# Optimization experiments

Measured on AMD Instinct MI355X. Metric: run time of the kernel, lower is better.

The kernel has to match this reference:

```python
import jax, jax.numpy as jnp
import numpy as np

N_NODES = 100000
N_EDGES = 1600000
F_IN = 64
HIDDEN = 64
N_CLASSES = 2


def setup_inputs() -> dict:
    key = jax.random.key(0)
    k1, k2, k3, k4, k5, k6 = jax.random.split(key, 6)
    x = jax.random.normal(k1, (N_NODES, F_IN), dtype=jnp.float32)
    edge_index = jax.random.randint(k2, (2, N_EDGES), 0, N_NODES, dtype=jnp.int64)
    # Glorot-ish init for GCNConv linear weights, zero bias (PyG default)
    W1 = jax.random.normal(k3, (F_IN, HIDDEN), dtype=jnp.float32) * (1.0 / np.sqrt(F_IN))
    b1 = jnp.zeros((HIDDEN,), dtype=jnp.float32)
    W2 = jax.random.normal(k4, (HIDDEN, N_CLASSES), dtype=jnp.float32) * (1.0 / np.sqrt(HIDDEN))
    b2 = jnp.zeros((N_CLASSES,), dtype=jnp.float32)
    return {"x": x, "edge_index": edge_index, "W1": W1, "b1": b1, "W2": W2, "b2": b2}


def _gcn_norm(edge_index, num_nodes):
    # Add self-loops, then symmetric normalization D^-1/2 (A+I) D^-1/2
    loops = jnp.arange(num_nodes, dtype=edge_index.dtype)
    row = jnp.concatenate([edge_index[0], loops])  # [E+N] targets
    col = jnp.concatenate([edge_index[1], loops])  # [E+N] sources
    deg = jax.ops.segment_sum(jnp.ones(row.shape[0], jnp.float32), row, num_segments=num_nodes)
    dinv = jnp.where(deg > 0, jax.lax.rsqrt(deg), 0.0)
    norm = dinv[row] * dinv[col]  # [E+N]
    return row, col, norm


def _gcn_conv(x, W, b, row, col, norm, num_nodes):
    h = x @ W                                   # [N, out]
    msg = h[col] * norm[:, None]                # gather + scale, [E+N, out]
    agg = jax.ops.segment_sum(msg, row, num_segments=num_nodes)  # scatter-add
    return agg + b


def reference(x, edge_index, W1, b1, W2, b2):
    n = x.shape[0]
    row, col, norm = _gcn_norm(edge_index, n)
    h = jax.nn.relu(_gcn_conv(x, W1, b1, row, col, norm, n))
    # dropout p=0.5 is identity in eval mode
    logits = _gcn_conv(h, W2, b2, row, col, norm, n)
    return jax.nn.softmax(logits, axis=1)
```

## Files before the change

### kernel.cpp

```cpp
#include <hip/hip_runtime.h>
#include <hip/hip_fp16.h>


typedef _Float16 f16x8 __attribute__((ext_vector_type(8)));
typedef float f32x4 __attribute__((ext_vector_type(4)));
typedef float f32x2 __attribute__((ext_vector_type(2)));

#define CAPSH 12
#define CAP (1 << CAPSH)
#define NBK 784

__device__ __forceinline__ unsigned char pack_fp8(float v) {
    return (unsigned char)(__builtin_amdgcn_cvt_pk_fp8_f32(v, 0.f, 0, false) & 0xFF);
}

__device__ __forceinline__ void unpack8_fp8(uint2 w, float* f) {
    f32x2 a = __builtin_amdgcn_cvt_pk_f32_fp8(w.x, false);
    f32x2 b = __builtin_amdgcn_cvt_pk_f32_fp8(w.x, true);
    f32x2 c = __builtin_amdgcn_cvt_pk_f32_fp8(w.y, false);
    f32x2 d = __builtin_amdgcn_cvt_pk_f32_fp8(w.y, true);
    f[0] = a.x; f[1] = a.y; f[2] = b.x; f[3] = b.y;
    f[4] = c.x; f[5] = c.y; f[6] = d.x; f[7] = d.y;
}

__global__ __launch_bounds__(256, 4) void k_binfused(const int* __restrict__ row,
                                                     const int* __restrict__ col,
                                                     int* __restrict__ relcur,
                                                     unsigned* __restrict__ pairbuf,
                                                     unsigned char* __restrict__ hp8,
                                                     const float* __restrict__ x,
                                                     const float* __restrict__ W1,
                                                     int E, int nb, int N, int nTileB) {
    __shared__ unsigned items[4096];
    __shared__ unsigned short bktid[4096];
    __shared__ int cnt[NBK];
    __shared__ int start0[NBK];
    __shared__ int cursor[NBK];
    __shared__ int gbase[NBK];

    int tid = threadIdx.x;

    if (blockIdx.x < nTileB) {
        int base = blockIdx.x * 4096;
        int m = E - base; if (m > 4096) m = 4096;

        for (int t = tid; t < nb; t += 256) cnt[t] = 0;
        __syncthreads();
        for (int i = tid; i < m; i += 256) atomicAdd(&cnt[row[base + i] >> 7], 1);
        __syncthreads();
        if (tid < 64) {
            int lane = tid, running = 0;
            for (int ch = 0; ch < 13; ++ch) {
                int idx = ch * 64 + lane;
                int v = (idx < nb) ? cnt[idx] : 0;
                int s = v;
#pragma unroll
                for (int off = 1; off < 64; off <<= 1) {
                    int t = __shfl_up(s, off, 64);
                    if (lane >= off) s += t;
                }
                if (idx < nb) { start0[idx] = running + s - v; cursor[idx] = running + s - v; }
                running += __shfl(s, 63, 64);
            }
        }
        __syncthreads();
        for (int i = tid; i < m; i += 256) {
            int r = row[base + i];
            int c = col[base + i];
            int b = r >> 7;
            int pos = atomicAdd(&cursor[b], 1);
            items[pos] = ((unsigned)(r & 127) << 24) | (unsigned)c;
            bktid[pos] = (unsigned short)b;
        }
        __syncthreads();
        for (int t = tid; t < nb; t += 256) {
            int cv = cnt[t];
            if (cv > 0) gbase[t] = (t << CAPSH) + atomicAdd(&relcur[t], cv);
        }
        __syncthreads();
        for (int i = tid; i < m; i += 256) {
            int b = bktid[i];
            pairbuf[gbase[b] + (i - start0[b])] = items[i];
        }
        if (blockIdx.x == 0 && tid < 16) ((int*)(hp8 + (size_t)N * 64))[tid] = 0;
    } else {
        int g = blockIdx.x - nTileB;
        int n0 = g << 8;
        int lane = tid & 63, q = lane >> 4, mm = lane & 15;
        f16x8 bf[4][2];
#pragma unroll
        for (int nt = 0; nt < 4; ++nt)
#pragma unroll
            for (int kk = 0; kk < 2; ++kk)
#pragma unroll
                for (int j = 0; j < 8; ++j)
                    bf[nt][kk][j] = (_Float16)W1[(kk * 32 + q * 8 + j) * 64 + nt * 16 + mm];

        int nn = N - n0; if (nn > 256) nn = 256;
        for (int t = (tid >> 6); t < (nn >> 4); t += 4) {
            const float* xrow = x + (size_t)(n0 + t * 16 + mm) * 64;
            float4 u0 = *(const float4*)(xrow + q * 8);
            float4 u1 = *(const float4*)(xrow + q * 8 + 4);
            float4 u2 = *(const float4*)(xrow + 32 + q * 8);
            float4 u3 = *(const float4*)(xrow + 32 + q * 8 + 4);
            f16x8 a0, a1;
            a0[0] = (_Float16)u0.x; a0[1] = (_Float16)u0.y; a0[2] = (_Float16)u0.z; a0[3] = (_Float16)u0.w;
            a0[4] = (_Float16)u1.x; a0[5] = (_Float16)u1.y; a0[6] = (_Float16)u1.z; a0[7] = (_Float16)u1.w;
            a1[0] = (_Float16)u2.x; a1[1] = (_Float16)u2.y; a1[2] = (_Float16)u2.z; a1[3] = (_Float16)u2.w;
            a1[4] = (_Float16)u3.x; a1[5] = (_Float16)u3.y; a1[6] = (_Float16)u3.z; a1[7] = (_Float16)u3.w;
            f32x4 ac0 = {0.f, 0.f, 0.f, 0.f}, ac1 = ac0, ac2 = ac0, ac3 = ac0;
            ac0 = __builtin_amdgcn_mfma_f32_16x16x32_f16(a0, bf[0][0], ac0, 0, 0, 0);
            ac1 = __builtin_amdgcn_mfma_f32_16x16x32_f16(a0, bf[1][0], ac1, 0, 0, 0);
            ac2 = __builtin_amdgcn_mfma_f32_16x16x32_f16(a0, bf[2][0], ac2, 0, 0, 0);
            ac3 = __builtin_amdgcn_mfma_f32_16x16x32_f16(a0, bf[3][0], ac3, 0, 0, 0);
            ac0 = __builtin_amdgcn_mfma_f32_16x16x32_f16(a1, bf[0][1], ac0, 0, 0, 0);
            ac1 = __builtin_amdgcn_mfma_f32_16x16x32_f16(a1, bf[1][1], ac1, 0, 0, 0);
            ac2 = __builtin_amdgcn_mfma_f32_16x16x32_f16(a1, bf[2][1], ac2, 0, 0, 0);
            ac3 = __builtin_amdgcn_mfma_f32_16x16x32_f16(a1, bf[3][1], ac3, 0, 0, 0);
#pragma unroll
            for (int reg = 0; reg < 4; ++reg) {
                int rl = t * 16 + q * 4 + reg;
                unsigned char* dst = hp8 + (size_t)(n0 + rl) * 64 + mm;
                dst[0]  = pack_fp8(ac0[reg]);
                dst[16] = pack_fp8(ac1[reg]);
                dst[32] = pack_fp8(ac2[reg]);
                dst[48] = pack_fp8(ac3[reg]);
            }
        }
    }
}

__global__ __launch_bounds__(256, 4) void k_sort(const unsigned* __restrict__ pairbuf,
                                                 const int* __restrict__ relcur,
                                                 int* __restrict__ scol,
                                                 int* __restrict__ offsets,
                                                 int* __restrict__ deg,
                                                 float* __restrict__ dinv,
                                                 int N, int nb) {
    __shared__ int cnt[256];
    __shared__ int spre[128];
    __shared__ int cur[128];
    int b = blockIdx.x;
    int tid = threadIdx.x;
    int lo = b << CAPSH;
    int hi = lo + relcur[b];
    cnt[tid] = 0;
    __syncthreads();
    for (int i = lo + tid; i < hi; i += 256)
        atomicAdd(&cnt[pairbuf[i] >> 24], 1);
    __syncthreads();
    if (tid < 64) {
        int lane = tid, running = 0;
#pragma unroll
        for (int ch = 0; ch < 2; ++ch) {
            int idx = ch * 64 + lane;
            int v = cnt[idx];
            int s = v;
#pragma unroll
            for (int off = 1; off < 64; off <<= 1) {
                int t = __shfl_up(s, off, 64);
                if (lane >= off) s += t;
            }
            spre[idx] = running + s - v;
            running += __shfl(s, 63, 64);
        }
    }
    __syncthreads();
    int n0 = b << 7;
    if (tid < 128) {
        int cv = cnt[tid];
        int excl = spre[tid];
        int n = n0 + tid;
        if (n < N) {
            offsets[n] = lo + excl;
            deg[n] = cv;
            dinv[n] = rsqrtf((float)(cv + 1));
        }
        cur[tid] = lo + excl;
    }
    if (b == 0 && tid == 0) {
        offsets[N] = 0; deg[N] = 0;
        dinv[N] = 0.f;
        scol[nb << CAPSH] = N;
    }
    __syncthreads();
    for (int i = lo + tid; i < hi; i += 256) {
        unsigned it = pairbuf[i];
        int pos = atomicAdd(&cur[it >> 24], 1);
        scol[pos] = (int)(it & 0xFFFFFFu);
    }
}

__global__ __launch_bounds__(256, 4) void k_agg1(const unsigned char* __restrict__ hp8,
                                                 const int* __restrict__ offsets,
                                                 const int* __restrict__ deg,
                                                 const int* __restrict__ scol,
                                                 const float* __restrict__ dinv,
                                                 const float* __restrict__ b1,
                                                 const float* __restrict__ W2,
                                                 float2* __restrict__ h2p,
                                                 int N, int SENT) {
    int lane = threadIdx.x & 63;
    int slot = lane >> 3;
    int chunk = lane & 7;
    int wid = (int)((blockIdx.x * 256 + threadIdx.x) >> 6);
    int n = wid * 8 + slot;
    int nc = (n < N) ? n : N;
    int start = offsets[nc];
    int dg = deg[nc];
    int maxd = dg;
#pragma unroll
    for (int s = 8; s <= 32; s <<= 1) {
        int o = __shfl_xor(maxd, s, 64);
        maxd = (o > maxd) ? o : maxd;
    }
    const uint2* hp2 = (const uint2*)hp8;
    float dn = dinv[(n < N) ? n : (N - 1)];
    float af[8];
    {
        uint2 sr = hp2[(size_t)nc * 8 + chunk];
        float fs[8];
        unpack8_fp8(sr, fs);
#pragma unroll
        for (int k = 0; k < 8; ++k) af[k] = dn * fs[k];
    }
    for (int j0 = 0; j0 < maxd; j0 += 8) {
        int c[8];
#pragma unroll
        for (int u = 0; u < 8; ++u)
            c[u] = scol[(j0 + u < dg) ? (start + j0 + u) : SENT];
        uint2 r[8];
#pragma unroll
        for (int u = 0; u < 8; ++u) r[u] = hp2[(size_t)c[u] * 8 + chunk];
        float dv[8];
#pragma unroll
        for (int u = 0; u < 8; ++u) dv[u] = dinv[c[u]];
#pragma unroll
        for (int u = 0; u < 8; ++u) {
            float f[8];
            unpack8_fp8(r[u], f);
#pragma unroll
            for (int k = 0; k < 8; ++k)
                af[k] = fmaf(dv[u], f[k], af[k]);
        }
    }
    float4 b1a = ((const float4*)b1)[chunk * 2];
    float4 b1b = ((const float4*)b1)[chunk * 2 + 1];
    float h1[8];
    h1[0] = fmaxf(fmaf(dn, af[0], b1a.x), 0.f);
    h1[1] = fmaxf(fmaf(dn, af[1], b1a.y), 0.f);
    h1[2] = fmaxf(fmaf(dn, af[2], b1a.z), 0.f);
    h1[3] = fmaxf(fmaf(dn, af[3], b1a.w), 0.f);
    h1[4] = fmaxf(fmaf(dn, af[4], b1b.x), 0.f);
    h1[5] = fmaxf(fmaf(dn, af[5], b1b.y), 0.f);
    h1[6] = fmaxf(fmaf(dn, af[6], b1b.z), 0.f);
    h1[7] = fmaxf(fmaf(dn, af[7], b1b.w), 0.f);
    float p0 = 0.f, p1 = 0.f;
#pragma unroll
    for (int k = 0; k < 4; ++k) {
        float4 w = ((const float4*)W2)[chunk * 4 + k];
        p0 = fmaf(h1[2 * k], w.x, p0); p1 = fmaf(h1[2 * k], w.y, p1);
        p0 = fmaf(h1[2 * k + 1], w.z, p0); p1 = fmaf(h1[2 * k + 1], w.w, p1);
    }
#pragma unroll
    for (int s = 1; s <= 4; s <<= 1) {
        p0 += __shfl_xor(p0, s, 64);
        p1 += __shfl_xor(p1, s, 64);
    }
    if (chunk == 0 && n < N) h2p[n] = make_float2(dn * p0, dn * p1);
}

__global__ __launch_bounds__(256) void k_agg2(const float2* __restrict__ h2p,
                                              const int* __restrict__ offsets,
                                              const int* __restrict__ deg,
                                              const int* __restrict__ scol,
                                              const float* __restrict__ dinv,
                                              const float* __restrict__ b2,
                                              float2* __restrict__ out, int N) {
    int gtid = blockIdx.x * 256 + threadIdx.x;
    int n = gtid >> 4;
    int sub = threadIdx.x & 15;
    if (n >= N) return;
    int start = offsets[n], end = start + deg[n];
    float ax = 0.f, ay = 0.f;
    if (sub == 0) { float2 s = h2p[n]; ax = s.x; ay = s.y; }
    for (int j = start + sub; j < end; j += 16) {
        float2 v = h2p[scol[j]];
        ax += v.x; ay += v.y;
    }
#pragma unroll
    for (int s = 1; s <= 8; s <<= 1) {
        ax += __shfl_xor(ax, s, 64);
        ay += __shfl_xor(ay, s, 64);
    }
    if (sub == 0) {
        float dn = dinv[n];
        float l0 = fmaf(dn, ax, b2[0]), l1 = fmaf(dn, ay, b2[1]);
        float m = fmaxf(l0, l1);
        float e0 = __expf(l0 - m), e1 = __expf(l1 - m);
        float inv = 1.0f / (e0 + e1);
        out[n] = make_float2(e0 * inv, e1 * inv);
    }
}

extern "C" void kernel_launch(void* const* d_in, const int* in_sizes, int n_in,
                              void* d_out, int out_size, void* d_ws, size_t ws_size,
                              hipStream_t stream) {
    const float* x  = (const float*)d_in[0];
    const int*   ei = (const int*)d_in[1];
    const float* W1 = (const float*)d_in[2];
    const float* b1 = (const float*)d_in[3];
    const float* W2 = (const float*)d_in[4];
    const float* b2 = (const float*)d_in[5];
    float2* out = (float2*)d_out;

    const int N = in_sizes[0] / 64;
    const int E = in_sizes[1] / 2;
    const int nb = (N + 127) >> 7;
    const int SENT = nb << CAPSH;
    const int* row = ei;
    const int* col = ei + E;

    char* p = (char*)d_ws;
    auto alloc = [&](size_t bytes) -> void* {
        void* r = (void*)p;
        p += (bytes + 255) & ~(size_t)255;
        return r;
    };
    int*   relcur  = (int*)alloc((size_t)nb * 4);
    int*   offsets = (int*)alloc((size_t)(N + 1) * 4);
    int*   deg     = (int*)alloc((size_t)(N + 1) * 4);
    float* dinv    = (float*)alloc((size_t)(N + 1) * 4);
    unsigned* pairbuf = (unsigned*)alloc((size_t)nb * CAP * 4);
    int*   scol    = (int*)alloc(((size_t)nb * CAP + 1) * 4);
    unsigned char* hp8 = (unsigned char*)alloc((size_t)(N + 1) * 64);
    float2* h2p    = (float2*)alloc((size_t)N * 8);

    const int nTileB = (E + 4095) / 4096;
    const int nGemm  = (N + 255) >> 8;

    hipMemsetAsync(relcur, 0, (size_t)nb * 4, stream);
    k_binfused<<<nTileB + nGemm, 256, 0, stream>>>(row, col, relcur, pairbuf, hp8,
                                                   x, W1, E, nb, N, nTileB);
    k_sort<<<nb, 256, 0, stream>>>(pairbuf, relcur, scol, offsets, deg, dinv, N, nb);
    const int nwaves = (N + 7) / 8;
    k_agg1<<<(nwaves + 3) / 4, 256, 0, stream>>>(hp8, offsets, deg, scol, dinv, b1, W2, h2p, N, SENT);
    k_agg2<<<(N * 16 + 255) / 256, 256, 0, stream>>>(h2p, offsets, deg, scol, dinv, b2, out, N);
}
```

Measured before the change: 161.9 us.

## Fuse all stages into one cooperative persistent kernel with grid syncs

```diff
diff --git a/kernel.cpp b/kernel.cpp
--- a/kernel.cpp
+++ b/kernel.cpp
@@ -1,5 +1,8 @@
 #include <hip/hip_runtime.h>
 #include <hip/hip_fp16.h>
+#include <hip/hip_cooperative_groups.h>
+
+namespace cg = cooperative_groups;
 
 
 typedef _Float16 f16x8 __attribute__((ext_vector_type(8)));
@@ -23,14 +26,25 @@
     f[4] = c.x; f[5] = c.y; f[6] = d.x; f[7] = d.y;
 }
 
-__global__ __launch_bounds__(256, 4) void k_binfused(const int* __restrict__ row,
-                                                     const int* __restrict__ col,
-                                                     int* __restrict__ relcur,
-                                                     unsigned* __restrict__ pairbuf,
-                                                     unsigned char* __restrict__ hp8,
-                                                     const float* __restrict__ x,
-                                                     const float* __restrict__ W1,
-                                                     int E, int nb, int N, int nTileB) {
+__global__ __launch_bounds__(256, 4) void k_mega(const int* __restrict__ row,
+                                                 const int* __restrict__ col,
+                                                 int* __restrict__ relcur,
+                                                 unsigned* __restrict__ pairbuf,
+                                                 unsigned char* __restrict__ hp8,
+                                                 const float* __restrict__ x,
+                                                 const float* __restrict__ W1,
+                                                 int* __restrict__ scol,
+                                                 int* __restrict__ offsets,
+                                                 int* __restrict__ deg,
+                                                 float* __restrict__ dinv,
+                                                 const float* __restrict__ b1,
+                                                 const float* __restrict__ W2,
+                                                 float2* __restrict__ h2p,
+                                                 const float* __restrict__ b2,
+                                                 float2* __restrict__ out,
+                                                 int E, int nb, int N, int nTileB, int SENT) {
+    cg::grid_group grid = cg::this_grid();
+
     __shared__ unsigned items[4096];
     __shared__ unsigned short bktid[4096];
     __shared__ int cnt[NBK];
@@ -38,268 +52,259 @@
     __shared__ int cursor[NBK];
     __shared__ int gbase[NBK];
 
-    int tid = threadIdx.x;
-
-    if (blockIdx.x < nTileB) {
-        int base = blockIdx.x * 4096;
-        int m = E - base; if (m > 4096) m = 4096;
-
-        for (int t = tid; t < nb; t += 256) cnt[t] = 0;
-        __syncthreads();
-        for (int i = tid; i < m; i += 256) atomicAdd(&cnt[row[base + i] >> 7], 1);
+    const int tid = threadIdx.x;
+    const int bid = blockIdx.x;
+    const int G = gridDim.x;
+
+    for (int t = bid * 256 + tid; t < nb; t += G * 256) relcur[t] = 0;
+    if (bid == 0 && tid < 16) ((int*)(hp8 + (size_t)N * 64))[tid] = 0;
+    grid.sync();
+
+    const int nGemm = (N + 255) >> 8;
+    for (int bb = bid; bb < nTileB + nGemm; bb += G) {
+        if (bb < nTileB) {
+            int base = bb * 4096;
+            int m = E - base; if (m > 4096) m = 4096;
+
+            for (int t = tid; t < nb; t += 256) cnt[t] = 0;
+            __syncthreads();
+            for (int i = tid; i < m; i += 256) atomicAdd(&cnt[row[base + i] >> 7], 1);
+            __syncthreads();
+            if (tid < 64) {
+                int lane = tid, running = 0;
+                for (int ch = 0; ch < 13; ++ch) {
+                    int idx = ch * 64 + lane;
+                    int v = (idx < nb) ? cnt[idx] : 0;
+                    int s = v;
+#pragma unroll
+                    for (int off = 1; off < 64; off <<= 1) {
+                        int t2 = __shfl_up(s, off, 64);
+                        if (lane >= off) s += t2;
+                    }
+                    if (idx < nb) { start0[idx] = running + s - v; cursor[idx] = running + s - v; }
+                    running += __shfl(s, 63, 64);
+                }
+            }
+            __syncthreads();
+            for (int i = tid; i < m; i += 256) {
+                int r = row[base + i];
+                int c = col[base + i];
+                int b = r >> 7;
+                int pos = atomicAdd(&cursor[b], 1);
+                items[pos] = ((unsigned)(r & 127) << 24) | (unsigned)c;
+                bktid[pos] = (unsigned short)b;
+            }
+            __syncthreads();
+            for (int t = tid; t < nb; t += 256) {
+                int cv = cnt[t];
+                if (cv > 0) gbase[t] = (t << CAPSH) + atomicAdd(&relcur[t], cv);
+            }
+            __syncthreads();
+            for (int i = tid; i < m; i += 256) {
+                int b = bktid[i];
+                pairbuf[gbase[b] + (i - start0[b])] = items[i];
+            }
+            __syncthreads();
+        } else {
+            int g = bb - nTileB;
+            int n0 = g << 8;
+            int lane = tid & 63, q = lane >> 4, mm = lane & 15;
+            f16x8 bf[4][2];
+#pragma unroll
+            for (int nt = 0; nt < 4; ++nt)
+#pragma unroll
+                for (int kk = 0; kk < 2; ++kk)
+#pragma unroll
+                    for (int j = 0; j < 8; ++j)
+                        bf[nt][kk][j] = (_Float16)W1[(kk * 32 + q * 8 + j) * 64 + nt * 16 + mm];
+
+            int nn = N - n0; if (nn > 256) nn = 256;
+            for (int t = (tid >> 6); t < (nn >> 4); t += 4) {
+                const float* xrow = x + (size_t)(n0 + t * 16 + mm) * 64;
+                float4 u0 = *(const float4*)(xrow + q * 8);
+                float4 u1 = *(const float4*)(xrow + q * 8 + 4);
+                float4 u2 = *(const float4*)(xrow + 32 + q * 8);
+                float4 u3 = *(const float4*)(xrow + 32 + q * 8 + 4);
+                f16x8 a0, a1;
+                a0[0] = (_Float16)u0.x; a0[1] = (_Float16)u0.y; a0[2] = (_Float16)u0.z; a0[3] = (_Float16)u0.w;
+                a0[4] = (_Float16)u1.x; a0[5] = (_Float16)u1.y; a0[6] = (_Float16)u1.z; a0[7] = (_Float16)u1.w;
+                a1[0] = (_Float16)u2.x; a1[1] = (_Float16)u2.y; a1[2] = (_Float16)u2.z; a1[3] = (_Float16)u2.w;
+                a1[4] = (_Float16)u3.x; a1[5] = (_Float16)u3.y; a1[6] = (_Float16)u3.z; a1[7] = (_Float16)u3.w;
+                f32x4 ac0 = {0.f, 0.f, 0.f, 0.f}, ac1 = ac0, ac2 = ac0, ac3 = ac0;
+                ac0 = __builtin_amdgcn_mfma_f32_16x16x32_f16(a0, bf[0][0], ac0, 0, 0, 0);
+                ac1 = __builtin_amdgcn_mfma_f32_16x16x32_f16(a0, bf[1][0], ac1, 0, 0, 0);
+                ac2 = __builtin_amdgcn_mfma_f32_16x16x32_f16(a0, bf[2][0], ac2, 0, 0, 0);
+                ac3 = __builtin_amdgcn_mfma_f32_16x16x32_f16(a0, bf[3][0], ac3, 0, 0, 0);
+                ac0 = __builtin_amdgcn_mfma_f32_16x16x32_f16(a1, bf[0][1], ac0, 0, 0, 0);
+                ac1 = __builtin_amdgcn_mfma_f32_16x16x32_f16(a1, bf[1][1], ac1, 0, 0, 0);
+                ac2 = __builtin_amdgcn_mfma_f32_16x16x32_f16(a1, bf[2][1], ac2, 0, 0, 0);
+                ac3 = __builtin_amdgcn_mfma_f32_16x16x32_f16(a1, bf[3][1], ac3, 0, 0, 0);
+#pragma unroll
+                for (int reg = 0; reg < 4; ++reg) {
+                    int rl = t * 16 + q * 4 + reg;
+                    unsigned char* dst = hp8 + (size_t)(n0 + rl) * 64 + mm;
+                    dst[0]  = pack_fp8(ac0[reg]);
+                    dst[16] = pack_fp8(ac1[reg]);
+                    dst[32] = pack_fp8(ac2[reg]);
+                    dst[48] = pack_fp8(ac3[reg]);
+                }
+            }
+        }
+    }
+    grid.sync();
+
+    for (int b = bid; b < nb; b += G) {
+        int lo = b << CAPSH;
+        int hi = lo + relcur[b];
+        cnt[tid] = 0;
+        __syncthreads();
+        for (int i = lo + tid; i < hi; i += 256)
+            atomicAdd(&cnt[pairbuf[i] >> 24], 1);
         __syncthreads();
         if (tid < 64) {
             int lane = tid, running = 0;
-            for (int ch = 0; ch < 13; ++ch) {
+#pragma unroll
+            for (int ch = 0; ch < 2; ++ch) {
                 int idx = ch * 64 + lane;
-                int v = (idx < nb) ? cnt[idx] : 0;
+                int v = cnt[idx];
                 int s = v;
 #pragma unroll
                 for (int off = 1; off < 64; off <<= 1) {
-                    int t = __shfl_up(s, off, 64);
-                    if (lane >= off) s += t;
+                    int t2 = __shfl_up(s, off, 64);
+                    if (lane >= off) s += t2;
                 }
-                if (idx < nb) { start0[idx] = running + s - v; cursor[idx] = running + s - v; }
+                start0[idx] = running + s - v;
                 running += __shfl(s, 63, 64);
             }
         }
         __syncthreads();
-        for (int i = tid; i < m; i += 256) {
-            int r = row[base + i];
-            int c = col[base + i];
-            int b = r >> 7;
-            int pos = atomicAdd(&cursor[b], 1);
-            items[pos] = ((unsigned)(r & 127) << 24) | (unsigned)c;
-            bktid[pos] = (unsigned short)b;
-        }
-        __syncthreads();
-        for (int t = tid; t < nb; t += 256) {
-            int cv = cnt[t];
-            if (cv > 0) gbase[t] = (t << CAPSH) + atomicAdd(&relcur[t], cv);
-        }
-        __syncthreads();
-        for (int i = tid; i < m; i += 256) {
-            int b = bktid[i];
-            pairbuf[gbase[b] + (i - start0[b])] = items[i];
-        }
-        if (blockIdx.x == 0 && tid < 16) ((int*)(hp8 + (size_t)N * 64))[tid] = 0;
-    } else {
-        int g = blockIdx.x - nTileB;
-        int n0 = g << 8;
-        int lane = tid & 63, q = lane >> 4, mm = lane & 15;
-        f16x8 bf[4][2];
-#pragma unroll
-        for (int nt = 0; nt < 4; ++nt)
-#pragma unroll
-            for (int kk = 0; kk < 2; ++kk)
-#pragma unroll
-                for (int j = 0; j < 8; ++j)
-                    bf[nt][kk][j] = (_Float16)W1[(kk * 32 + q * 8 + j) * 64 + nt * 16 + mm];
-
-        int nn = N - n0; if (nn > 256) nn = 256;
-        for (int t = (tid >> 6); t < (nn >> 4); t += 4) {
-            const float* xrow = x + (size_t)(n0 + t * 16 + mm) * 64;
-            float4 u0 = *(const float4*)(xrow + q * 8);
-            float4 u1 = *(const float4*)(xrow + q * 8 + 4);
-            float4 u2 = *(const float4*)(xrow + 32 + q * 8);
-            float4 u3 = *(const float4*)(xrow + 32 + q * 8 + 4);
-            f16x8 a0, a1;
-            a0[0] = (_Float16)u0.x; a0[1] = (_Float16)u0.y; a0[2] = (_Float16)u0.z; a0[3] = (_Float16)u0.w;
-            a0[4] = (_Float16)u1.x; a0[5] = (_Float16)u1.y; a0[6] = (_Float16)u1.z; a0[7] = (_Float16)u1.w;
-            a1[0] = (_Float16)u2.x; a1[1] = (_Float16)u2.y; a1[2] = (_Float16)u2.z; a1[3] = (_Float16)u2.w;
-            a1[4] = (_Float16)u3.x; a1[5] = (_Float16)u3.y; a1[6] = (_Float16)u3.z; a1[7] = (_Float16)u3.w;
-            f32x4 ac0 = {0.f, 0.f, 0.f, 0.f}, ac1 = ac0, ac2 = ac0, ac3 = ac0;
-            ac0 = __builtin_amdgcn_mfma_f32_16x16x32_f16(a0, bf[0][0], ac0, 0, 0, 0);
-            ac1 = __builtin_amdgcn_mfma_f32_16x16x32_f16(a0, bf[1][0], ac1, 0, 0, 0);
-            ac2 = __builtin_amdgcn_mfma_f32_16x16x32_f16(a0, bf[2][0], ac2, 0, 0, 0);
-            ac3 = __builtin_amdgcn_mfma_f32_16x16x32_f16(a0, bf[3][0], ac3, 0, 0, 0);
-            ac0 = __builtin_amdgcn_mfma_f32_16x16x32_f16(a1, bf[0][1], ac0, 0, 0, 0);
-            ac1 = __builtin_amdgcn_mfma_f32_16x16x32_f16(a1, bf[1][1], ac1, 0, 0, 0);
-            ac2 = __builtin_amdgcn_mfma_f32_16x16x32_f16(a1, bf[2][1], ac2, 0, 0, 0);
-            ac3 = __builtin_amdgcn_mfma_f32_16x16x32_f16(a1, bf[3][1], ac3, 0, 0, 0);
-#pragma unroll
-            for (int reg = 0; reg < 4; ++reg) {
-                int rl = t * 16 + q * 4 + reg;
-                unsigned char* dst = hp8 + (size_t)(n0 + rl) * 64 + mm;
-                dst[0]  = pack_fp8(ac0[reg]);
-                dst[16] = pack_fp8(ac1[reg]);
-                dst[32] = pack_fp8(ac2[reg]);
-                dst[48] = pack_fp8(ac3[reg]);
-            }
-        }
-    }
-}
-
-__global__ __launch_bounds__(256, 4) void k_sort(const unsigned* __restrict__ pairbuf,
-                                                 const int* __restrict__ relcur,
-                                                 int* __restrict__ scol,
-                                                 int* __restrict__ offsets,
-                                                 int* __restrict__ deg,
-                                                 float* __restrict__ dinv,
-                                                 int N, int nb) {
-    __shared__ int cnt[256];
-    __shared__ int spre[128];
-    __shared__ int cur[128];
-    int b = blockIdx.x;
-    int tid = threadIdx.x;
-    int lo = b << CAPSH;
-    int hi = lo + relcur[b];
-    cnt[tid] = 0;
-    __syncthreads();
-    for (int i = lo + tid; i < hi; i += 256)
-        atomicAdd(&cnt[pairbuf[i] >> 24], 1);
-    __syncthreads();
-    if (tid < 64) {
-        int lane = tid, running = 0;
-#pragma unroll
-        for (int ch = 0; ch < 2; ++ch) {
-            int idx = ch * 64 + lane;
-            int v = cnt[idx];
-            int s = v;
-#pragma unroll
-            for (int off = 1; off < 64; off <<= 1) {
-                int t = __shfl_up(s, off, 64);
-                if (lane >= off) s += t;
-            }
-            spre[idx] = running + s - v;
-            running += __shfl(s, 63, 64);
-        }
-    }
-    __syncthreads();
-    int n0 = b << 7;
-    if (tid < 128) {
-        int cv = cnt[tid];
-        int excl = spre[tid];
-        int n = n0 + tid;
-        if (n < N) {
-            offsets[n] = lo + excl;
-            deg[n] = cv;
-            dinv[n] = rsqrtf((float)(cv + 1));
-        }
-        cur[tid] = lo + excl;
-    }
-    if (b == 0 && tid == 0) {
-        offsets[N] = 0; deg[N] = 0;
-        dinv[N] = 0.f;
-        scol[nb << CAPSH] = N;
-    }
-    __syncthreads();
-    for (int i = lo + tid; i < hi; i += 256) {
-        unsigned it = pairbuf[i];
-        int pos = atomicAdd(&cur[it >> 24], 1);
-        scol[pos] = (int)(it & 0xFFFFFFu);
-    }
-}
-
-__global__ __launch_bounds__(256, 4) void k_agg1(const unsigned char* __restrict__ hp8,
-                                                 const int* __restrict__ offsets,
-                                                 const int* __restrict__ deg,
-                                                 const int* __restrict__ scol,
-                                                 const float* __restrict__ dinv,
-                                                 const float* __restrict__ b1,
-                                                 const float* __restrict__ W2,
-                                                 float2* __restrict__ h2p,
-                                                 int N, int SENT) {
-    int lane = threadIdx.x & 63;
-    int slot = lane >> 3;
-    int chunk = lane & 7;
-    int wid = (int)((blockIdx.x * 256 + threadIdx.x) >> 6);
-    int n = wid * 8 + slot;
-    int nc = (n < N) ? n : N;
-    int start = offsets[nc];
-    int dg = deg[nc];
-    int maxd = dg;
-#pragma unroll
-    for (int s = 8; s <= 32; s <<= 1) {
-        int o = __shfl_xor(maxd, s, 64);
-        maxd = (o > maxd) ? o : maxd;
-    }
-    const uint2* hp2 = (const uint2*)hp8;
-    float dn = dinv[(n < N) ? n : (N - 1)];
-    float af[8];
+        int n0 = b << 7;
+        if (tid < 128) {
+            int cv = cnt[tid];
+            int excl = start0[tid];
+            int n = n0 + tid;
+            if (n < N) {
+                offsets[n] = lo + excl;
+                deg[n] = cv;
+                dinv[n] = rsqrtf((float)(cv + 1));
+            }
+            cursor[tid] = lo + excl;
+        }
+        if (b == 0 && tid == 0) {
+            offsets[N] = 0; deg[N] = 0;
+            dinv[N] = 0.f;
+            scol[nb << CAPSH] = N;
+        }
+        __syncthreads();
+        for (int i = lo + tid; i < hi; i += 256) {
+            unsigned it = pairbuf[i];
+            int pos = atomicAdd(&cursor[it >> 24], 1);
+            scol[pos] = (int)(it & 0xFFFFFFu);
+        }
+        __syncthreads();
+    }
+    grid.sync();
+
     {
-        uint2 sr = hp2[(size_t)nc * 8 + chunk];
-        float fs[8];
-        unpack8_fp8(sr, fs);
-#pragma unroll
-        for (int k = 0; k < 8; ++k) af[k] = dn * fs[k];
-    }
-    for (int j0 = 0; j0 < maxd; j0 += 8) {
-        int c[8];
-#pragma unroll
-        for (int u = 0; u < 8; ++u)
-            c[u] = scol[(j0 + u < dg) ? (start + j0 + u) : SENT];
-        uint2 r[8];
-#pragma unroll
-        for (int u = 0; u < 8; ++u) r[u] = hp2[(size_t)c[u] * 8 + chunk];
-        float dv[8];
-#pragma unroll
-        for (int u = 0; u < 8; ++u) dv[u] = dinv[c[u]];
-#pragma unroll
-        for (int u = 0; u < 8; ++u) {
-            float f[8];
-            unpack8_fp8(r[u], f);
-#pragma unroll
-            for (int k = 0; k < 8; ++k)
-                af[k] = fmaf(dv[u], f[k], af[k]);
-        }
-    }
-    float4 b1a = ((const float4*)b1)[chunk * 2];
-    float4 b1b = ((const float4*)b1)[chunk * 2 + 1];
-    float h1[8];
-    h1[0] = fmaxf(fmaf(dn, af[0], b1a.x), 0.f);
-    h1[1] = fmaxf(fmaf(dn, af[1], b1a.y), 0.f);
-    h1[2] = fmaxf(fmaf(dn, af[2], b1a.z), 0.f);
-    h1[3] = fmaxf(fmaf(dn, af[3], b1a.w), 0.f);
-    h1[4] = fmaxf(fmaf(dn, af[4], b1b.x), 0.f);
-    h1[5] = fmaxf(fmaf(dn, af[5], b1b.y), 0.f);
-    h1[6] = fmaxf(fmaf(dn, af[6], b1b.z), 0.f);
-    h1[7] = fmaxf(fmaf(dn, af[7], b1b.w), 0.f);
-    float p0 = 0.f, p1 = 0.f;
-#pragma unroll
-    for (int k = 0; k < 4; ++k) {
-        float4 w = ((const float4*)W2)[chunk * 4 + k];
-        p0 = fmaf(h1[2 * k], w.x, p0); p1 = fmaf(h1[2 * k], w.y, p1);
-        p0 = fmaf(h1[2 * k + 1], w.z, p0); p1 = fmaf(h1[2 * k + 1], w.w, p1);
-    }
-#pragma unroll
-    for (int s = 1; s <= 4; s <<= 1) {
-        p0 += __shfl_xor(p0, s, 64);
-        p1 += __shfl_xor(p1, s, 64);
-    }
-    if (chunk == 0 && n < N) h2p[n] = make_float2(dn * p0, dn * p1);
-}
-
-__global__ __launch_bounds__(256) void k_agg2(const float2* __restrict__ h2p,
-                                              const int* __restrict__ offsets,
-                                              const int* __restrict__ deg,
-                                              const int* __restrict__ scol,
-                                              const float* __restrict__ dinv,
-                                              const float* __restrict__ b2,
-                                              float2* __restrict__ out, int N) {
-    int gtid = blockIdx.x * 256 + threadIdx.x;
-    int n = gtid >> 4;
-    int sub = threadIdx.x & 15;
-    if (n >= N) return;
-    int start = offsets[n], end = start + deg[n];
-    float ax = 0.f, ay = 0.f;
-    if (sub == 0) { float2 s = h2p[n]; ax = s.x; ay = s.y; }
-    for (int j = start + sub; j < end; j += 16) {
-        float2 v = h2p[scol[j]];
-        ax += v.x; ay += v.y;
-    }
-#pragma unroll
-    for (int s = 1; s <= 8; s <<= 1) {
-        ax += __shfl_xor(ax, s, 64);
-        ay += __shfl_xor(ay, s, 64);
-    }
-    if (sub == 0) {
-        float dn = dinv[n];
-        float l0 = fmaf(dn, ax, b2[0]), l1 = fmaf(dn, ay, b2[1]);
-        float m = fmaxf(l0, l1);
-        float e0 = __expf(l0 - m), e1 = __expf(l1 - m);
-        float inv = 1.0f / (e0 + e1);
-        out[n] = make_float2(e0 * inv, e1 * inv);
+        int lane = tid & 63;
+        int slot = lane >> 3;
+        int chunk = lane & 7;
+        int nwaves = (N + 7) >> 3;
+        const uint2* hp2 = (const uint2*)hp8;
+        for (int wid = (bid * 256 + tid) >> 6; wid < nwaves; wid += G * 4) {
+            int n = wid * 8 + slot;
+            int nc = (n < N) ? n : N;
+            int start = offsets[nc];
+            int dg = deg[nc];
+            int maxd = dg;
+#pragma unroll
+            for (int s = 8; s <= 32; s <<= 1) {
+                int o = __shfl_xor(maxd, s, 64);
+                maxd = (o > maxd) ? o : maxd;
+            }
+            float dn = dinv[(n < N) ? n : (N - 1)];
+            float af[8];
+            {
+                uint2 sr = hp2[(size_t)nc * 8 + chunk];
+                float fs[8];
+                unpack8_fp8(sr, fs);
+#pragma unroll
+                for (int k = 0; k < 8; ++k) af[k] = dn * fs[k];
+            }
+            for (int j0 = 0; j0 < maxd; j0 += 8) {
+                int c[8];
+#pragma unroll
+                for (int u = 0; u < 8; ++u)
+                    c[u] = scol[(j0 + u < dg) ? (start + j0 + u) : SENT];
+                uint2 r[8];
+#pragma unroll
+                for (int u = 0; u < 8; ++u) r[u] = hp2[(size_t)c[u] * 8 + chunk];
+                float dv[8];
+#pragma unroll
+                for (int u = 0; u < 8; ++u) dv[u] = dinv[c[u]];
+#pragma unroll
+                for (int u = 0; u < 8; ++u) {
+                    float f[8];
+                    unpack8_fp8(r[u], f);
+#pragma unroll
+                    for (int k = 0; k < 8; ++k)
+                        af[k] = fmaf(dv[u], f[k], af[k]);
+                }
+            }
+            float4 b1a = ((const float4*)b1)[chunk * 2];
+            float4 b1b = ((const float4*)b1)[chunk * 2 + 1];
+            float h1[8];
+            h1[0] = fmaxf(fmaf(dn, af[0], b1a.x), 0.f);
+            h1[1] = fmaxf(fmaf(dn, af[1], b1a.y), 0.f);
+            h1[2] = fmaxf(fmaf(dn, af[2], b1a.z), 0.f);
+            h1[3] = fmaxf(fmaf(dn, af[3], b1a.w), 0.f);
+            h1[4] = fmaxf(fmaf(dn, af[4], b1b.x), 0.f);
+            h1[5] = fmaxf(fmaf(dn, af[5], b1b.y), 0.f);
+            h1[6] = fmaxf(fmaf(dn, af[6], b1b.z), 0.f);
+            h1[7] = fmaxf(fmaf(dn, af[7], b1b.w), 0.f);
+            float p0 = 0.f, p1 = 0.f;
+#pragma unroll
+            for (int k = 0; k < 4; ++k) {
+                float4 w = ((const float4*)W2)[chunk * 4 + k];
+                p0 = fmaf(h1[2 * k], w.x, p0); p1 = fmaf(h1[2 * k], w.y, p1);
+                p0 = fmaf(h1[2 * k + 1], w.z, p0); p1 = fmaf(h1[2 * k + 1], w.w, p1);
+            }
+#pragma unroll
+            for (int s = 1; s <= 4; s <<= 1) {
+                p0 += __shfl_xor(p0, s, 64);
+                p1 += __shfl_xor(p1, s, 64);
+            }
+            if (chunk == 0 && n < N) h2p[n] = make_float2(dn * p0, dn * p1);
+        }
+    }
+    grid.sync();
+
+    {
+        float bb0 = b2[0], bb1 = b2[1];
+        for (int gtid = bid * 256 + tid; gtid < N * 16; gtid += G * 256) {
+            int n = gtid >> 4;
+            int sub = gtid & 15;
+            int start = offsets[n], end = start + deg[n];
+            float ax = 0.f, ay = 0.f;
+            if (sub == 0) { float2 s = h2p[n]; ax = s.x; ay = s.y; }
+            for (int j = start + sub; j < end; j += 16) {
+                float2 v = h2p[scol[j]];
+                ax += v.x; ay += v.y;
+            }
+#pragma unroll
+            for (int s = 1; s <= 8; s <<= 1) {
+                ax += __shfl_xor(ax, s, 64);
+                ay += __shfl_xor(ay, s, 64);
+            }
+            if (sub == 0) {
+                float dn = dinv[n];
+                float l0 = fmaf(dn, ax, bb0), l1 = fmaf(dn, ay, bb1);
+                float m = fmaxf(l0, l1);
+                float e0 = __expf(l0 - m), e1 = __expf(l1 - m);
+                float inv = 1.0f / (e0 + e1);
+                out[n] = make_float2(e0 * inv, e1 * inv);
+            }
+        }
     }
 }
 
@@ -338,12 +343,27 @@
 
     const int nTileB = (E + 4095) / 4096;
     const int nGemm  = (N + 255) >> 8;
-
-    hipMemsetAsync(relcur, 0, (size_t)nb * 4, stream);
-    k_binfused<<<nTileB + nGemm, 256, 0, stream>>>(row, col, relcur, pairbuf, hp8,
-                                                   x, W1, E, nb, N, nTileB);
-    k_sort<<<nb, 256, 0, stream>>>(pairbuf, relcur, scol, offsets, deg, dinv, N, nb);
-    const int nwaves = (N + 7) / 8;
-    k_agg1<<<(nwaves + 3) / 4, 256, 0, stream>>>(hp8, offsets, deg, scol, dinv, b1, W2, h2p, N, SENT);
-    k_agg2<<<(N * 16 + 255) / 256, 256, 0, stream>>>(h2p, offsets, deg, scol, dinv, b2, out, N);
+    int target = nTileB + nGemm;
+    if (nb > target) target = nb;
+
+    static int capBlocks = 0;
+    if (capBlocks == 0) {
+        int maxB = 0;
+        hipError_t e = hipOccupancyMaxActiveBlocksPerMultiprocessor(&maxB, (const void*)k_mega, 256, 0);
+        if (e != hipSuccess || maxB < 1) maxB = 2;
+        hipDeviceProp_t prop;
+        int dev = 0;
+        hipGetDevice(&dev);
+        if (hipGetDeviceProperties(&prop, dev) != hipSuccess) prop.multiProcessorCount = 256;
+        capBlocks = maxB * prop.multiProcessorCount;
+        if (capBlocks < 1) capBlocks = 256;
+    }
+    int G = (target < capBlocks) ? target : capBlocks;
+
+    int E_ = E, nb_ = nb, N_ = N, nTileB_ = nTileB, SENT_ = SENT;
+    void* args[] = { (void*)&row, (void*)&col, (void*)&relcur, (void*)&pairbuf, (void*)&hp8,
+                     (void*)&x, (void*)&W1, (void*)&scol, (void*)&offsets, (void*)&deg,
+                     (void*)&dinv, (void*)&b1, (void*)&W2, (void*)&h2p, (void*)&b2,
+                     (void*)&out, (void*)&E_, (void*)&nb_, (void*)&N_, (void*)&nTileB_, (void*)&SENT_ };
+    hipLaunchCooperativeKernel((const void*)k_mega, dim3(G), dim3(256), args, 0, stream);
 }
```

Result: slower. 444.1 us (+174.3%).

## Degree-sort nodes for agg1 load balance and reduce layer-2 to logit difference

Applied to the files above, without the earlier changes.

```diff
diff --git a/kernel.cpp b/kernel.cpp
--- a/kernel.cpp
+++ b/kernel.cpp
@@ -56,8 +56,8 @@
                 int s = v;
 #pragma unroll
                 for (int off = 1; off < 64; off <<= 1) {
-                    int t = __shfl_up(s, off, 64);
-                    if (lane >= off) s += t;
+                    int t2 = __shfl_up(s, off, 64);
+                    if (lane >= off) s += t2;
                 }
                 if (idx < nb) { start0[idx] = running + s - v; cursor[idx] = running + s - v; }
                 running += __shfl(s, 63, 64);
@@ -136,6 +136,7 @@
                                                  int* __restrict__ offsets,
                                                  int* __restrict__ deg,
                                                  float* __restrict__ dinv,
+                                                 int* __restrict__ ord,
                                                  int N, int nb) {
     __shared__ int cnt[256];
     __shared__ int spre[128];
@@ -158,8 +159,8 @@
             int s = v;
 #pragma unroll
             for (int off = 1; off < 64; off <<= 1) {
-                int t = __shfl_up(s, off, 64);
-                if (lane >= off) s += t;
+                int t2 = __shfl_up(s, off, 64);
+                if (lane >= off) s += t2;
             }
             spre[idx] = running + s - v;
             running += __shfl(s, 63, 64);
@@ -189,6 +190,36 @@
         int pos = atomicAdd(&cur[it >> 24], 1);
         scol[pos] = (int)(it & 0xFFFFFFu);
     }
+    __syncthreads();
+    if (tid < 128) spre[tid] = 0;
+    __syncthreads();
+    int binv = 0;
+    if (tid < 128) {
+        binv = cnt[tid]; if (binv > 127) binv = 127;
+        atomicAdd(&spre[binv], 1);
+    }
+    __syncthreads();
+    if (tid < 64) {
+        int lane = tid, running = 0;
+#pragma unroll
+        for (int ch = 0; ch < 2; ++ch) {
+            int idx = ch * 64 + lane;
+            int v = spre[idx];
+            int s = v;
+#pragma unroll
+            for (int off = 1; off < 64; off <<= 1) {
+                int t2 = __shfl_up(s, off, 64);
+                if (lane >= off) s += t2;
+            }
+            cur[idx] = running + s - v;
+            running += __shfl(s, 63, 64);
+        }
+    }
+    __syncthreads();
+    if (tid < 128) {
+        int pos = atomicAdd(&cur[binv], 1);
+        ord[(b << 7) + pos] = n0 + tid;
+    }
 }
 
 __global__ __launch_bounds__(256, 4) void k_agg1(const unsigned char* __restrict__ hp8,
@@ -196,15 +227,18 @@
                                                  const int* __restrict__ deg,
                                                  const int* __restrict__ scol,
                                                  const float* __restrict__ dinv,
+                                                 const int* __restrict__ ord,
                                                  const float* __restrict__ b1,
                                                  const float* __restrict__ W2,
-                                                 float2* __restrict__ h2p,
-                                                 int N, int SENT) {
+                                                 float* __restrict__ h2pd,
+                                                 int N, int SENT, int nwaves) {
     int lane = threadIdx.x & 63;
     int slot = lane >> 3;
     int chunk = lane & 7;
     int wid = (int)((blockIdx.x * 256 + threadIdx.x) >> 6);
-    int n = wid * 8 + slot;
+    if (blockIdx.x == 0 && threadIdx.x == 0) h2pd[N] = 0.f;
+    if (wid >= nwaves) return;
+    int n = ord[wid * 8 + slot];
     int nc = (n < N) ? n : N;
     int start = offsets[nc];
     int dg = deg[nc];
@@ -215,7 +249,7 @@
         maxd = (o > maxd) ? o : maxd;
     }
     const uint2* hp2 = (const uint2*)hp8;
-    float dn = dinv[(n < N) ? n : (N - 1)];
+    float dn = dinv[nc];
     float af[8];
     {
         uint2 sr = hp2[(size_t)nc * 8 + chunk];
@@ -267,39 +301,39 @@
         p0 += __shfl_xor(p0, s, 64);
         p1 += __shfl_xor(p1, s, 64);
     }
-    if (chunk == 0 && n < N) h2p[n] = make_float2(dn * p0, dn * p1);
-}
-
-__global__ __launch_bounds__(256) void k_agg2(const float2* __restrict__ h2p,
+    if (chunk == 0 && n < N) h2pd[n] = dn * (p0 - p1);
+}
+
+__global__ __launch_bounds__(256) void k_agg2(const float* __restrict__ h2pd,
                                               const int* __restrict__ offsets,
                                               const int* __restrict__ deg,
                                               const int* __restrict__ scol,
                                               const float* __restrict__ dinv,
                                               const float* __restrict__ b2,
-                                              float2* __restrict__ out, int N) {
+                                              float2* __restrict__ out, int N, int SENT) {
     int gtid = blockIdx.x * 256 + threadIdx.x;
     int n = gtid >> 4;
     int sub = threadIdx.x & 15;
     if (n >= N) return;
     int start = offsets[n], end = start + deg[n];
     float ax = 0.f, ay = 0.f;
-    if (sub == 0) { float2 s = h2p[n]; ax = s.x; ay = s.y; }
-    for (int j = start + sub; j < end; j += 16) {
-        float2 v = h2p[scol[j]];
-        ax += v.x; ay += v.y;
-    }
-#pragma unroll
-    for (int s = 1; s <= 8; s <<= 1) {
+    if (sub == 0) ax = h2pd[n];
+    for (int j = start + sub; j < end; j += 32) {
+        int c0 = scol[j];
+        int c1 = (j + 16 < end) ? scol[j + 16] : SENT;
+        ax += h2pd[c0];
+        ay += h2pd[c1];
+    }
+    ax += ay;
+#pragma unroll
+    for (int s = 1; s <= 8; s <<= 1)
         ax += __shfl_xor(ax, s, 64);
-        ay += __shfl_xor(ay, s, 64);
-    }
     if (sub == 0) {
         float dn = dinv[n];
-        float l0 = fmaf(dn, ax, b2[0]), l1 = fmaf(dn, ay, b2[1]);
-        float m = fmaxf(l0, l1);
-        float e0 = __expf(l0 - m), e1 = __expf(l1 - m);
-        float inv = 1.0f / (e0 + e1);
-        out[n] = make_float2(e0 * inv, e1 * inv);
+        float ld = fmaf(dn, ax, b2[0] - b2[1]);
+        float e = __expf(-ld);
+        float inv = 1.0f / (1.0f + e);
+        out[n] = make_float2(inv, e * inv);
     }
 }
 
@@ -334,7 +368,8 @@
     unsigned* pairbuf = (unsigned*)alloc((size_t)nb * CAP * 4);
     int*   scol    = (int*)alloc(((size_t)nb * CAP + 1) * 4);
     unsigned char* hp8 = (unsigned char*)alloc((size_t)(N + 1) * 64);
-    float2* h2p    = (float2*)alloc((size_t)N * 8);
+    float* h2pd    = (float*)alloc((size_t)(N + 1) * 4);
+    int*   ord     = (int*)alloc((size_t)nb * 128 * 4);
 
     const int nTileB = (E + 4095) / 4096;
     const int nGemm  = (N + 255) >> 8;
@@ -342,8 +377,8 @@
     hipMemsetAsync(relcur, 0, (size_t)nb * 4, stream);
     k_binfused<<<nTileB + nGemm, 256, 0, stream>>>(row, col, relcur, pairbuf, hp8,
                                                    x, W1, E, nb, N, nTileB);
-    k_sort<<<nb, 256, 0, stream>>>(pairbuf, relcur, scol, offsets, deg, dinv, N, nb);
-    const int nwaves = (N + 7) / 8;
-    k_agg1<<<(nwaves + 3) / 4, 256, 0, stream>>>(hp8, offsets, deg, scol, dinv, b1, W2, h2p, N, SENT);
-    k_agg2<<<(N * 16 + 255) / 256, 256, 0, stream>>>(h2p, offsets, deg, scol, dinv, b2, out, N);
-}
+    k_sort<<<nb, 256, 0, stream>>>(pairbuf, relcur, scol, offsets, deg, dinv, ord, N, nb);
+    const int nwaves = nb * 16;
+    k_agg1<<<nb * 4, 256, 0, stream>>>(hp8, offsets, deg, scol, dinv, ord, b1, W2, h2pd, N, SENT, nwaves);
+    k_agg2<<<(N * 16 + 255) / 256, 256, 0, stream>>>(h2pd, offsets, deg, scol, dinv, b2, out, N, SENT);
+}
```

New measurement: 163.8 us. About the same (+1.2%).
